# Performance work log

Hardware: AMD Instinct MI355X
Metric: run time of the kernel (lower is better)

Reference implementation:

```python
import jax, jax.numpy as jnp
import numpy as np

N, IN_C, OUT_C = 4096, 256, 64
ALPHA = 0.2  # LeakyReLU negative slope


def setup_inputs() -> dict:
    key = jax.random.key(0)
    k1, k2, k3, k4 = jax.random.split(key, 4)
    H = jax.random.normal(k1, (N, IN_C), dtype=jnp.float32)
    adj = jax.random.randint(k2, (N, N), 0, 2, dtype=jnp.int32)
    # xavier_uniform with gain=1.414
    gain = 1.414
    limW = gain * np.sqrt(6.0 / (IN_C + OUT_C))
    W = jax.random.uniform(k3, (IN_C, OUT_C), minval=-limW, maxval=limW, dtype=jnp.float32)
    lima = gain * np.sqrt(6.0 / (2 * OUT_C + 1))
    a = jax.random.uniform(k4, (2 * OUT_C, 1), minval=-lima, maxval=lima, dtype=jnp.float32)
    return {"H": H, "adj": adj, "W": W, "a": a}


def reference(H, adj, W, a):
    Wh = H @ W  # [N, out_C]
    # Attention_Mat[i,j] = concat(Wh_i, Wh_j); score = Attention_Mat @ a
    # = (Wh @ a1)_i + (Wh @ a2)_j  -- fused, avoids the O(N^2 * 2F) tensor.
    a1, a2 = a[:OUT_C, 0], a[OUT_C:, 0]
    e = (Wh @ a1)[:, None] + (Wh @ a2)[None, :]  # [N, N]
    e = jnp.where(e > 0, e, ALPHA * e)  # LeakyReLU
    att = jax.nn.softmax(e, axis=1)
    # NOTE: original masks AFTER softmax (rows are not renormalized).
    att = jnp.where(adj > 0, att, jnp.zeros_like(att))
    out = att @ Wh  # [N, out_C]
    return jax.nn.elu(out)  # concat=True
```

## Files before the change

### kernel.cpp

```cpp
#include <hip/hip_runtime.h>
#include <math.h>

static constexpr int NN   = 4096;
static constexpr int INC  = 256;
static constexpr int OUTC = 64;

typedef _Float16 half8 __attribute__((ext_vector_type(8)));
typedef float floatx4 __attribute__((ext_vector_type(4)));

#if __has_builtin(__builtin_amdgcn_exp2f)
#define EXP2F(x) __builtin_amdgcn_exp2f(x)
#else
#define EXP2F(x) exp2f(x)
#endif

__device__ __forceinline__ float lrelu(float x) {
    return fmaxf(x, 0.2f * x);
}
__device__ __forceinline__ float elu1(float x) {
    return x > 0.f ? x : (__expf(x) - 1.f);
}

__global__ __launch_bounds__(256) void k_prep(const int* __restrict__ adj,
                                              unsigned int* __restrict__ bits,
                                              const float* __restrict__ H,
                                              const float* __restrict__ W,
                                              const float* __restrict__ a,
                                              unsigned short* __restrict__ WhT,
                                              float* __restrict__ f1,
                                              float* __restrict__ f2) {
    __shared__ __align__(16) float Hl[16 * INC];
    __shared__ _Float16 Tl[16 * 68];
    const int t = threadIdx.x;
    if (blockIdx.x >= 256) {
        unsigned char* nib = (unsigned char*)Hl;
        const int blk = blockIdx.x - 256;
        const int4* src = (const int4*)adj + (size_t)blk * 2048;
        #pragma unroll
        for (int k = 0; k < 8; ++k) {
            const int4 v = src[k * 256 + t];
            nib[k * 256 + t] = (unsigned char)((unsigned int)(v.x > 0)
                             | ((unsigned int)(v.y > 0) << 1)
                             | ((unsigned int)(v.z > 0) << 2)
                             | ((unsigned int)(v.w > 0) << 3));
        }
        __syncthreads();
        const unsigned int* n32 = (const unsigned int*)nib;
        unsigned int lo = n32[t * 2 + 0];
        unsigned int hi = n32[t * 2 + 1];
        lo |= lo >> 4;  lo &= 0x00FF00FFu;  lo |= lo >> 8;  lo &= 0x0000FFFFu;
        hi |= hi >> 4;  hi &= 0x00FF00FFu;  hi |= hi >> 8;  hi &= 0x0000FFFFu;
        bits[blk * 256 + t] = lo | (hi << 16);
        return;
    }
    const int i0 = blockIdx.x * 16;
    {
        const float4* H4 = (const float4*)(H + i0 * INC);
        float4* Hl4 = (float4*)Hl;
        #pragma unroll
        for (int u = 0; u < 4; ++u) Hl4[u * 256 + t] = H4[u * 256 + t];
    }
    __syncthreads();
    const int c = t & 63;
    const int g = t >> 6;
    const float a1c = a[c];
    const float a2c = a[OUTC + c];
    float acc[4] = {0.f, 0.f, 0.f, 0.f};
    const float4* Hl4 = (const float4*)Hl;
    #pragma unroll 4
    for (int k4 = 0; k4 < INC / 4; ++k4) {
        const float w0 = W[(k4 * 4 + 0) * OUTC + c];
        const float w1 = W[(k4 * 4 + 1) * OUTC + c];
        const float w2 = W[(k4 * 4 + 2) * OUTC + c];
        const float w3 = W[(k4 * 4 + 3) * OUTC + c];
        #pragma unroll
        for (int s = 0; s < 4; ++s) {
            const float4 h = Hl4[(g + 4 * s) * (INC / 4) + k4];
            acc[s] = fmaf(h.x, w0, fmaf(h.y, w1, fmaf(h.z, w2, fmaf(h.w, w3, acc[s]))));
        }
    }
    #pragma unroll
    for (int s = 0; s < 4; ++s) {
        const int r = g + 4 * s;
        Tl[r * 68 + c] = (_Float16)acc[s];
        float v1 = acc[s] * a1c;
        float v2 = acc[s] * a2c;
        #pragma unroll
        for (int off = 32; off; off >>= 1) {
            v1 += __shfl_xor(v1, off);
            v2 += __shfl_xor(v2, off);
        }
        if (c == 0) { f1[i0 + r] = v1; f2[i0 + r] = v2; }
    }
    __syncthreads();
    const int c2 = t >> 2;
    const int rs = (t & 3) * 4;
    ushort4 u;
    u.x = *(const unsigned short*)&Tl[(rs + 0) * 68 + c2];
    u.y = *(const unsigned short*)&Tl[(rs + 1) * 68 + c2];
    u.z = *(const unsigned short*)&Tl[(rs + 2) * 68 + c2];
    u.w = *(const unsigned short*)&Tl[(rs + 3) * 68 + c2];
    *(ushort4*)(WhT + c2 * NN + i0 + rs) = u;
}

__global__ __launch_bounds__(1024, 4) void k_att(const unsigned char* __restrict__ bits,
                                                 const _Float16* __restrict__ WhT,
                                                 const float* __restrict__ f1,
                                                 const float* __restrict__ f2,
                                                 float* __restrict__ out) {
    __shared__ __align__(16) float sf2[NN];
    __shared__ __align__(16) float sacc[16 * 1024];
    __shared__ float sden[16 * 16];
    __shared__ float smax[16];
    const int t = threadIdx.x;
    const int w = t >> 6;
    const int l = t & 63;
    const int m = l & 15;
    const int quad = l >> 4;
    const int i0 = blockIdx.x * 16;

    {
        const float4 v = ((const float4*)f2)[t];
        ((float4*)sf2)[t] = v;
        float mloc = fmaxf(fmaxf(v.x, v.y), fmaxf(v.z, v.w));
        #pragma unroll
        for (int off = 32; off; off >>= 1) mloc = fmaxf(mloc, __shfl_xor(mloc, off));
        if (l == 0) smax[w] = mloc;
    }
    __syncthreads();
    float maxf2 = smax[0];
    #pragma unroll
    for (int k = 1; k < 16; ++k) maxf2 = fmaxf(maxf2, smax[k]);

    const float f1r = f1[i0 + m];
    const float mrow = lrelu(f1r + maxf2);
    const float LOG2E = 1.44269504f;
    const float nm2 = -mrow * LOG2E;
    float den0 = 0.f, den1 = 0.f;
    floatx4 acc[4] = {{0.f,0.f,0.f,0.f},{0.f,0.f,0.f,0.f},{0.f,0.f,0.f,0.f},{0.f,0.f,0.f,0.f}};
    const int jbase = w * 32 + quad * 8;
    const unsigned char* brow = bits + (size_t)(i0 + m) * (NN / 8) + (jbase >> 3);
    unsigned int m8[8];
    #pragma unroll
    for (int it = 0; it < 8; ++it) m8[it] = brow[it * 64];

    #pragma unroll 2
    for (int it = 0; it < 8; ++it) {
        const int j = jbase + it * 512;
        const unsigned int mb = m8[it];
        const float4 g0 = *(const float4*)(sf2 + j);
        const float4 g1 = *(const float4*)(sf2 + j + 4);
        half8 af;
        {
            float z, p;
            z = f1r + g0.x; p = EXP2F(fmaf(fmaxf(z, 0.2f*z), LOG2E, nm2)); den0 += p; af[0] = (mb & 1u)   ? (_Float16)p : (_Float16)0.f;
            z = f1r + g0.y; p = EXP2F(fmaf(fmaxf(z, 0.2f*z), LOG2E, nm2)); den1 += p; af[1] = (mb & 2u)   ? (_Float16)p : (_Float16)0.f;
            z = f1r + g0.z; p = EXP2F(fmaf(fmaxf(z, 0.2f*z), LOG2E, nm2)); den0 += p; af[2] = (mb & 4u)   ? (_Float16)p : (_Float16)0.f;
            z = f1r + g0.w; p = EXP2F(fmaf(fmaxf(z, 0.2f*z), LOG2E, nm2)); den1 += p; af[3] = (mb & 8u)   ? (_Float16)p : (_Float16)0.f;
            z = f1r + g1.x; p = EXP2F(fmaf(fmaxf(z, 0.2f*z), LOG2E, nm2)); den0 += p; af[4] = (mb & 16u)  ? (_Float16)p : (_Float16)0.f;
            z = f1r + g1.y; p = EXP2F(fmaf(fmaxf(z, 0.2f*z), LOG2E, nm2)); den1 += p; af[5] = (mb & 32u)  ? (_Float16)p : (_Float16)0.f;
            z = f1r + g1.z; p = EXP2F(fmaf(fmaxf(z, 0.2f*z), LOG2E, nm2)); den0 += p; af[6] = (mb & 64u)  ? (_Float16)p : (_Float16)0.f;
            z = f1r + g1.w; p = EXP2F(fmaf(fmaxf(z, 0.2f*z), LOG2E, nm2)); den1 += p; af[7] = (mb & 128u) ? (_Float16)p : (_Float16)0.f;
        }
        #pragma unroll
        for (int nt = 0; nt < 4; ++nt) {
            const half8 bf = *(const half8*)(WhT + (size_t)(nt * 16 + m) * NN + j);
            acc[nt] = __builtin_amdgcn_mfma_f32_16x16x32_f16(af, bf, acc[nt], 0, 0, 0);
        }
    }
    float den = den0 + den1;
    den += __shfl_xor(den, 16);
    den += __shfl_xor(den, 32);
    if (l < 16) sden[w * 16 + l] = den;
    #pragma unroll
    for (int nt = 0; nt < 4; ++nt)
        #pragma unroll
        for (int r = 0; r < 4; ++r)
            sacc[w * 1024 + (quad * 4 + r) * 64 + nt * 16 + m] = acc[nt][r];
    __syncthreads();
    float s = 0.f;
    #pragma unroll
    for (int w2 = 0; w2 < 16; ++w2) s += sacc[w2 * 1024 + t];
    float dden = 0.f;
    const int row = t >> 6;
    #pragma unroll
    for (int w2 = 0; w2 < 16; ++w2) dden += sden[w2 * 16 + row];
    out[(size_t)i0 * OUTC + t] = elu1(s / dden);
}

extern "C" void kernel_launch(void* const* d_in, const int* in_sizes, int n_in,
                              void* d_out, int out_size, void* d_ws, size_t ws_size,
                              hipStream_t stream) {
    const float* H  = (const float*)d_in[0];
    const int* adj  = (const int*)d_in[1];
    const float* W  = (const float*)d_in[2];
    const float* a  = (const float*)d_in[3];
    float* out = (float*)d_out;
    char* ws = (char*)d_ws;
    unsigned short* WhT = (unsigned short*)(ws);
    float* f1 = (float*)(ws + (512 << 10));
    float* f2 = (float*)(ws + (528 << 10));
    unsigned int* bits = (unsigned int*)(ws + (1 << 20));
    hipLaunchKernelGGL(k_prep, dim3(2304), dim3(256), 0, stream,
                       adj, bits, H, W, a, WhT, f1, f2);
    hipLaunchKernelGGL(k_att,  dim3(256),  dim3(1024), 0, stream,
                       (const unsigned char*)bits, (const _Float16*)WhT, f1, f2, out);
}
```

Baseline: 122.1 us.

## Read int32 adjacency directly in attention kernel instead of pre-packing bitmask

Removes the adjacency-to-bitmask packing blocks from the prep kernel and instead has the attention kernel read the int32 adjacency rows directly. Each thread prefetches its next 8 ints (two int4) one iteration ahead, and the main loop is now fully unrolled. This removes one full pass over the 64MB adjacency plus the bitmask write and read. In exchange, the attention kernel, which has only 256 blocks, must itself stream the full adjacency, so it may become bandwidth bound.

```diff
diff --git a/kernel.cpp b/kernel.cpp
--- a/kernel.cpp
+++ b/kernel.cpp
@@ -21,9 +21,7 @@
     return x > 0.f ? x : (__expf(x) - 1.f);
 }
 
-__global__ __launch_bounds__(256) void k_prep(const int* __restrict__ adj,
-                                              unsigned int* __restrict__ bits,
-                                              const float* __restrict__ H,
+__global__ __launch_bounds__(256) void k_prep(const float* __restrict__ H,
                                               const float* __restrict__ W,
                                               const float* __restrict__ a,
                                               unsigned short* __restrict__ WhT,
@@ -32,27 +30,6 @@
     __shared__ __align__(16) float Hl[16 * INC];
     __shared__ _Float16 Tl[16 * 68];
     const int t = threadIdx.x;
-    if (blockIdx.x >= 256) {
-        unsigned char* nib = (unsigned char*)Hl;
-        const int blk = blockIdx.x - 256;
-        const int4* src = (const int4*)adj + (size_t)blk * 2048;
-        #pragma unroll
-        for (int k = 0; k < 8; ++k) {
-            const int4 v = src[k * 256 + t];
-            nib[k * 256 + t] = (unsigned char)((unsigned int)(v.x > 0)
-                             | ((unsigned int)(v.y > 0) << 1)
-                             | ((unsigned int)(v.z > 0) << 2)
-                             | ((unsigned int)(v.w > 0) << 3));
-        }
-        __syncthreads();
-        const unsigned int* n32 = (const unsigned int*)nib;
-        unsigned int lo = n32[t * 2 + 0];
-        unsigned int hi = n32[t * 2 + 1];
-        lo |= lo >> 4;  lo &= 0x00FF00FFu;  lo |= lo >> 8;  lo &= 0x0000FFFFu;
-        hi |= hi >> 4;  hi &= 0x00FF00FFu;  hi |= hi >> 8;  hi &= 0x0000FFFFu;
-        bits[blk * 256 + t] = lo | (hi << 16);
-        return;
-    }
     const int i0 = blockIdx.x * 16;
     {
         const float4* H4 = (const float4*)(H + i0 * INC);
@@ -103,7 +80,7 @@
     *(ushort4*)(WhT + c2 * NN + i0 + rs) = u;
 }
 
-__global__ __launch_bounds__(1024, 4) void k_att(const unsigned char* __restrict__ bits,
+__global__ __launch_bounds__(1024, 4) void k_att(const int* __restrict__ adj,
                                                  const _Float16* __restrict__ WhT,
                                                  const float* __restrict__ f1,
                                                  const float* __restrict__ f2,
@@ -139,15 +116,27 @@
     float den0 = 0.f, den1 = 0.f;
     floatx4 acc[4] = {{0.f,0.f,0.f,0.f},{0.f,0.f,0.f,0.f},{0.f,0.f,0.f,0.f},{0.f,0.f,0.f,0.f}};
     const int jbase = w * 32 + quad * 8;
-    const unsigned char* brow = bits + (size_t)(i0 + m) * (NN / 8) + (jbase >> 3);
-    unsigned int m8[8];
+
+    const int4* arow = (const int4*)adj + (((size_t)(i0 + m) * NN + jbase) >> 2);
+    int4 p0 = arow[0];
+    int4 p1 = arow[1];
+
     #pragma unroll
-    for (int it = 0; it < 8; ++it) m8[it] = brow[it * 64];
-
-    #pragma unroll 2
     for (int it = 0; it < 8; ++it) {
         const int j = jbase + it * 512;
-        const unsigned int mb = m8[it];
+        int4 n0, n1;
+        if (it < 7) {
+            n0 = arow[(it + 1) * 128 + 0];
+            n1 = arow[(it + 1) * 128 + 1];
+        }
+        const unsigned int mb = (unsigned int)(p0.x > 0)
+                              | ((unsigned int)(p0.y > 0) << 1)
+                              | ((unsigned int)(p0.z > 0) << 2)
+                              | ((unsigned int)(p0.w > 0) << 3)
+                              | ((unsigned int)(p1.x > 0) << 4)
+                              | ((unsigned int)(p1.y > 0) << 5)
+                              | ((unsigned int)(p1.z > 0) << 6)
+                              | ((unsigned int)(p1.w > 0) << 7);
         const float4 g0 = *(const float4*)(sf2 + j);
         const float4 g1 = *(const float4*)(sf2 + j + 4);
         half8 af;
@@ -167,6 +156,7 @@
             const half8 bf = *(const half8*)(WhT + (size_t)(nt * 16 + m) * NN + j);
             acc[nt] = __builtin_amdgcn_mfma_f32_16x16x32_f16(af, bf, acc[nt], 0, 0, 0);
         }
+        p0 = n0; p1 = n1;
     }
     float den = den0 + den1;
     den += __shfl_xor(den, 16);
@@ -200,9 +190,8 @@
     unsigned short* WhT = (unsigned short*)(ws);
     float* f1 = (float*)(ws + (512 << 10));
     float* f2 = (float*)(ws + (528 << 10));
-    unsigned int* bits = (unsigned int*)(ws + (1 << 20));
-    hipLaunchKernelGGL(k_prep, dim3(2304), dim3(256), 0, stream,
-                       adj, bits, H, W, a, WhT, f1, f2);
+    hipLaunchKernelGGL(k_prep, dim3(256), dim3(256), 0, stream,
+                       H, W, a, WhT, f1, f2);
     hipLaunchKernelGGL(k_att,  dim3(256),  dim3(1024), 0, stream,
-                       (const unsigned char*)bits, (const _Float16*)WhT, f1, f2, out);
+                       adj, (const _Float16*)WhT, f1, f2, out);
 }
```

After: 128.6 us. +5.3%, slower.

## Split attention over four column chunks with last-block reduction and precomputed max

Applied to the files above, without the earlier changes.

The attention kernel now launches four 512-thread blocks per 16-row tile, each covering a quarter of the columns, instead of one 1024-thread block covering all columns. Partial numerators and denominators go to workspace, and the last-arriving block, found with an atomic counter, combines them and applies ELU. The global max of f2 is computed as per-block maxima in the prep kernel, so each attention block no longer scans all of f2, and the LeakyReLU/exp2 argument is folded algebraically to save an op per element. This aims to raise occupancy and balance across CUs, at the cost of extra global traffic for partials, plus fences and atomics.

```diff
diff --git a/kernel.cpp b/kernel.cpp
--- a/kernel.cpp
+++ b/kernel.cpp
@@ -14,9 +14,6 @@
 #define EXP2F(x) exp2f(x)
 #endif
 
-__device__ __forceinline__ float lrelu(float x) {
-    return fmaxf(x, 0.2f * x);
-}
 __device__ __forceinline__ float elu1(float x) {
     return x > 0.f ? x : (__expf(x) - 1.f);
 }
@@ -28,9 +25,12 @@
                                               const float* __restrict__ a,
                                               unsigned short* __restrict__ WhT,
                                               float* __restrict__ f1,
-                                              float* __restrict__ f2) {
+                                              float* __restrict__ f2,
+                                              float* __restrict__ blkmax,
+                                              unsigned int* __restrict__ cnt) {
     __shared__ __align__(16) float Hl[16 * INC];
     __shared__ _Float16 Tl[16 * 68];
+    __shared__ float wmax4[4];
     const int t = threadIdx.x;
     if (blockIdx.x >= 256) {
         unsigned char* nib = (unsigned char*)Hl;
@@ -53,6 +53,7 @@
         bits[blk * 256 + t] = lo | (hi << 16);
         return;
     }
+    if (t == 0) cnt[blockIdx.x] = 0;
     const int i0 = blockIdx.x * 16;
     {
         const float4* H4 = (const float4*)(H + i0 * INC);
@@ -79,6 +80,7 @@
             acc[s] = fmaf(h.x, w0, fmaf(h.y, w1, fmaf(h.z, w2, fmaf(h.w, w3, acc[s]))));
         }
     }
+    float vmax = -1e30f;
     #pragma unroll
     for (int s = 0; s < 4; ++s) {
         const int r = g + 4 * s;
@@ -90,9 +92,13 @@
             v1 += __shfl_xor(v1, off);
             v2 += __shfl_xor(v2, off);
         }
+        vmax = fmaxf(vmax, v2);
         if (c == 0) { f1[i0 + r] = v1; f2[i0 + r] = v2; }
     }
-    __syncthreads();
+    if (c == 0) wmax4[g] = vmax;
+    __syncthreads();
+    if (t == 0)
+        blkmax[blockIdx.x] = fmaxf(fmaxf(wmax4[0], wmax4[1]), fmaxf(wmax4[2], wmax4[3]));
     const int c2 = t >> 2;
     const int rs = (t & 3) * 4;
     ushort4 u;
@@ -103,64 +109,78 @@
     *(ushort4*)(WhT + c2 * NN + i0 + rs) = u;
 }
 
-__global__ __launch_bounds__(1024, 4) void k_att(const unsigned char* __restrict__ bits,
-                                                 const _Float16* __restrict__ WhT,
-                                                 const float* __restrict__ f1,
-                                                 const float* __restrict__ f2,
-                                                 float* __restrict__ out) {
-    __shared__ __align__(16) float sf2[NN];
-    __shared__ __align__(16) float sacc[16 * 1024];
-    __shared__ float sden[16 * 16];
-    __shared__ float smax[16];
+__global__ __launch_bounds__(512, 6) void k_att(const unsigned char* __restrict__ bits,
+                                                const _Float16* __restrict__ WhT,
+                                                const float* __restrict__ f1,
+                                                const float* __restrict__ f2,
+                                                const float* __restrict__ blkmax,
+                                                float* __restrict__ pout,
+                                                float* __restrict__ pden,
+                                                unsigned int* __restrict__ cnt,
+                                                float* __restrict__ out) {
+    __shared__ __align__(16) float sf2q[1024];
+    __shared__ __align__(16) float sacc[8 * 1024];
+    __shared__ float sden[8 * 16];
+    __shared__ float smax[8];
+    __shared__ unsigned int slast;
     const int t = threadIdx.x;
     const int w = t >> 6;
     const int l = t & 63;
     const int m = l & 15;
     const int quad = l >> 4;
-    const int i0 = blockIdx.x * 16;
+    const int tile = blockIdx.x >> 2;
+    const int q = blockIdx.x & 3;
+    const int i0 = tile * 16;
+    const float LOG2E = 1.44269504f;
 
     {
-        const float4 v = ((const float4*)f2)[t];
-        ((float4*)sf2)[t] = v;
-        float mloc = fmaxf(fmaxf(v.x, v.y), fmaxf(v.z, v.w));
+        float mloc = (t < 256) ? blkmax[t] : -1e30f;
         #pragma unroll
         for (int off = 32; off; off >>= 1) mloc = fmaxf(mloc, __shfl_xor(mloc, off));
         if (l == 0) smax[w] = mloc;
     }
+    if (t < 256) {
+        float4 v = ((const float4*)f2)[q * 256 + t];
+        v.x *= LOG2E; v.y *= LOG2E; v.z *= LOG2E; v.w *= LOG2E;
+        ((float4*)sf2q)[t] = v;
+    }
     __syncthreads();
     float maxf2 = smax[0];
     #pragma unroll
-    for (int k = 1; k < 16; ++k) maxf2 = fmaxf(maxf2, smax[k]);
+    for (int k = 1; k < 8; ++k) maxf2 = fmaxf(maxf2, smax[k]);
 
     const float f1r = f1[i0 + m];
-    const float mrow = lrelu(f1r + maxf2);
-    const float LOG2E = 1.44269504f;
+    const float zm = f1r + maxf2;
+    const float mrow = fmaxf(zm, 0.2f * zm);
     const float nm2 = -mrow * LOG2E;
+    const float f1c = fmaf(f1r, LOG2E, nm2);
+    const float c8 = 0.8f * nm2;
     float den0 = 0.f, den1 = 0.f;
     floatx4 acc[4] = {{0.f,0.f,0.f,0.f},{0.f,0.f,0.f,0.f},{0.f,0.f,0.f,0.f},{0.f,0.f,0.f,0.f}};
-    const int jbase = w * 32 + quad * 8;
-    const unsigned char* brow = bits + (size_t)(i0 + m) * (NN / 8) + (jbase >> 3);
-    unsigned int m8[8];
-    #pragma unroll
-    for (int it = 0; it < 8; ++it) m8[it] = brow[it * 64];
-
-    #pragma unroll 2
-    for (int it = 0; it < 8; ++it) {
-        const int j = jbase + it * 512;
-        const unsigned int mb = m8[it];
-        const float4 g0 = *(const float4*)(sf2 + j);
-        const float4 g1 = *(const float4*)(sf2 + j + 4);
+    const int jq = w * 32 + quad * 8;
+    const unsigned char* brow = bits + (size_t)(i0 + m) * (NN / 8) + ((q * 1024 + jq) >> 3);
+    unsigned int m4[4];
+    #pragma unroll
+    for (int it = 0; it < 4; ++it) m4[it] = brow[it * 32];
+
+    #pragma unroll
+    for (int it = 0; it < 4; ++it) {
+        const int jl = jq + it * 256;
+        const int j  = q * 1024 + jl;
+        const unsigned int mb = m4[it];
+        const float4 g0 = *(const float4*)(sf2q + jl);
+        const float4 g1 = *(const float4*)(sf2q + jl + 4);
         half8 af;
         {
-            float z, p;
-            z = f1r + g0.x; p = EXP2F(fmaf(fmaxf(z, 0.2f*z), LOG2E, nm2)); den0 += p; af[0] = (mb & 1u)   ? (_Float16)p : (_Float16)0.f;
-            z = f1r + g0.y; p = EXP2F(fmaf(fmaxf(z, 0.2f*z), LOG2E, nm2)); den1 += p; af[1] = (mb & 2u)   ? (_Float16)p : (_Float16)0.f;
-            z = f1r + g0.z; p = EXP2F(fmaf(fmaxf(z, 0.2f*z), LOG2E, nm2)); den0 += p; af[2] = (mb & 4u)   ? (_Float16)p : (_Float16)0.f;
-            z = f1r + g0.w; p = EXP2F(fmaf(fmaxf(z, 0.2f*z), LOG2E, nm2)); den1 += p; af[3] = (mb & 8u)   ? (_Float16)p : (_Float16)0.f;
-            z = f1r + g1.x; p = EXP2F(fmaf(fmaxf(z, 0.2f*z), LOG2E, nm2)); den0 += p; af[4] = (mb & 16u)  ? (_Float16)p : (_Float16)0.f;
-            z = f1r + g1.y; p = EXP2F(fmaf(fmaxf(z, 0.2f*z), LOG2E, nm2)); den1 += p; af[5] = (mb & 32u)  ? (_Float16)p : (_Float16)0.f;
-            z = f1r + g1.z; p = EXP2F(fmaf(fmaxf(z, 0.2f*z), LOG2E, nm2)); den0 += p; af[6] = (mb & 64u)  ? (_Float16)p : (_Float16)0.f;
-            z = f1r + g1.w; p = EXP2F(fmaf(fmaxf(z, 0.2f*z), LOG2E, nm2)); den1 += p; af[7] = (mb & 128u) ? (_Float16)p : (_Float16)0.f;
+            float u, p;
+            u = f1c + g0.x; p = EXP2F(fmaxf(u, fmaf(0.2f, u, c8))); den0 += p; af[0] = (mb & 1u)   ? (_Float16)p : (_Float16)0.f;
+            u = f1c + g0.y; p = EXP2F(fmaxf(u, fmaf(0.2f, u, c8))); den1 += p; af[1] = (mb & 2u)   ? (_Float16)p : (_Float16)0.f;
+            u = f1c + g0.z; p = EXP2F(fmaxf(u, fmaf(0.2f, u, c8))); den0 += p; af[2] = (mb & 4u)   ? (_Float16)p : (_Float16)0.f;
+            u = f1c + g0.w; p = EXP2F(fmaxf(u, fmaf(0.2f, u, c8))); den1 += p; af[3] = (mb & 8u)   ? (_Float16)p : (_Float16)0.f;
+            u = f1c + g1.x; p = EXP2F(fmaxf(u, fmaf(0.2f, u, c8))); den0 += p; af[4] = (mb & 16u)  ? (_Float16)p : (_Float16)0.f;
+            u = f1c + g1.y; p = EXP2F(fmaxf(u, fmaf(0.2f, u, c8))); den1 += p; af[5] = (mb & 32u)  ? (_Float16)p : (_Float16)0.f;
+            u = f1c + g1.z; p = EXP2F(fmaxf(u, fmaf(0.2f, u, c8))); den0 += p; af[6] = (mb & 64u)  ? (_Float16)p : (_Float16)0.f;
+            u = f1c + g1.w; p = EXP2F(fmaxf(u, fmaf(0.2f, u, c8))); den1 += p; af[7] = (mb & 128u) ? (_Float16)p : (_Float16)0.f;
         }
         #pragma unroll
         for (int nt = 0; nt < 4; ++nt) {
@@ -178,14 +198,41 @@
         for (int r = 0; r < 4; ++r)
             sacc[w * 1024 + (quad * 4 + r) * 64 + nt * 16 + m] = acc[nt][r];
     __syncthreads();
-    float s = 0.f;
-    #pragma unroll
-    for (int w2 = 0; w2 < 16; ++w2) s += sacc[w2 * 1024 + t];
-    float dden = 0.f;
-    const int row = t >> 6;
-    #pragma unroll
-    for (int w2 = 0; w2 < 16; ++w2) dden += sden[w2 * 16 + row];
-    out[(size_t)i0 * OUTC + t] = elu1(s / dden);
+    {
+        float s0 = 0.f, s1 = 0.f;
+        #pragma unroll
+        for (int w2 = 0; w2 < 8; ++w2) {
+            s0 += sacc[w2 * 1024 + t];
+            s1 += sacc[w2 * 1024 + t + 512];
+        }
+        pout[(size_t)tile * 4096 + q * 1024 + t]       = s0;
+        pout[(size_t)tile * 4096 + q * 1024 + t + 512] = s1;
+        if (t < 16) {
+            float d = 0.f;
+            #pragma unroll
+            for (int w2 = 0; w2 < 8; ++w2) d += sden[w2 * 16 + t];
+            pden[tile * 64 + q * 16 + t] = d;
+        }
+    }
+    __threadfence();
+    __syncthreads();
+    if (t == 0) slast = atomicAdd(&cnt[tile], 1u);
+    __syncthreads();
+    if (slast == 3u) {
+        __threadfence();
+        #pragma unroll
+        for (int half = 0; half < 2; ++half) {
+            const int o = t + half * 512;
+            const int row = o >> 6;
+            float v = 0.f, d = 0.f;
+            #pragma unroll
+            for (int q2 = 0; q2 < 4; ++q2) {
+                v += pout[(size_t)tile * 4096 + q2 * 1024 + o];
+                d += pden[tile * 64 + q2 * 16 + row];
+            }
+            out[(size_t)tile * 1024 + o] = elu1(v / d);
+        }
+    }
 }
 
 extern "C" void kernel_launch(void* const* d_in, const int* in_sizes, int n_in,
@@ -198,11 +245,16 @@
     float* out = (float*)d_out;
     char* ws = (char*)d_ws;
     unsigned short* WhT = (unsigned short*)(ws);
-    float* f1 = (float*)(ws + (512 << 10));
-    float* f2 = (float*)(ws + (528 << 10));
+    float* f1          = (float*)(ws + (512 << 10));
+    float* f2          = (float*)(ws + (528 << 10));
+    float* blkmax      = (float*)(ws + (544 << 10));
+    unsigned int* cnt  = (unsigned int*)(ws + (545 << 10));
+    float* pden        = (float*)(ws + (552 << 10));
     unsigned int* bits = (unsigned int*)(ws + (1 << 20));
+    float* pout        = (float*)(ws + (4 << 20));
     hipLaunchKernelGGL(k_prep, dim3(2304), dim3(256), 0, stream,
-                       adj, bits, H, W, a, WhT, f1, f2);
-    hipLaunchKernelGGL(k_att,  dim3(256),  dim3(1024), 0, stream,
-                       (const unsigned char*)bits, (const _Float16*)WhT, f1, f2, out);
-}
+                       adj, bits, H, W, a, WhT, f1, f2, blkmax, cnt);
+    hipLaunchKernelGGL(k_att,  dim3(1024), dim3(512), 0, stream,
+                       (const unsigned char*)bits, (const _Float16*)WhT, f1, f2,
+                       blkmax, pout, pden, cnt, out);
+}
```

After: 380.3 us. 3.12x slower.
